# Performance work log

Hardware: AMD Instinct MI355X
Metric: run time of the kernel (lower is better)

Reference implementation:

```python
import jax, jax.numpy as jnp
import numpy as np

N = 20000        # nodes per type
E = 320000       # edges per type (avg degree 16)
H = 8            # heads
F0 = 128         # initial feature dim
F_UNI = 256      # n_unified
F_OUT = 64       # n_units per layer
N_USER = 20000   # shape_ret[0]
N_CLASSES = 2


def setup_inputs() -> dict:
    key = jax.random.key(0)
    ks = jax.random.split(key, 32)
    nrm = lambda k, s: jax.random.normal(k, s, dtype=jnp.float32) * 0.05
    inp = {
        "hemb0": nrm(ks[0], (N, F0)),
        "hemb1": nrm(ks[1], (N, F0)),
        "W0": nrm(ks[2], (F0, F_UNI)),
        "W1": nrm(ks[3], (F0, F_UNI)),
    }
    i = 4
    for t in range(2):
        for l, fin in enumerate([F_UNI, H * F_OUT]):
            inp[f"g{t}l{l}_w"] = nrm(ks[i], (H, fin, F_OUT)); i += 1
            inp[f"g{t}l{l}_asrc"] = nrm(ks[i], (H, F_OUT)); i += 1
            inp[f"g{t}l{l}_atrg"] = nrm(ks[i], (H, F_OUT)); i += 1
    inp["aw1"] = nrm(ks[i], (F_UNI, F_OUT)); i += 1
    inp["aw2"] = nrm(ks[i], (F_OUT, F_OUT)); i += 1
    inp["am"] = nrm(ks[i], (F_OUT,)); i += 1
    inp["fc_w"] = nrm(ks[i], (F_OUT * 3, N_CLASSES)); i += 1
    inp["fc_b"] = jnp.zeros((N_CLASSES,), jnp.float32); i += 1
    inp["edge0"] = jax.random.randint(ks[i], (2, E), 0, N, dtype=jnp.int32); i += 1
    inp["edge1"] = jax.random.randint(ks[i], (2, E), 0, N, dtype=jnp.int32)
    return inp


def spgat(h, src, trg, w, asrc, atrg):
    """Sparse GAT layer: h [N,f_in], edge list src/trg [E] -> [N,H,f_out]."""
    n = h.shape[0]
    hp = jnp.einsum('nf,hfo->hno', h, w)              # [H,N,O]
    s = jnp.einsum('hno,ho->nh', hp, asrc)            # [N,H]
    t = jnp.einsum('hno,ho->nh', hp, atrg)            # [N,H]
    e = jax.nn.leaky_relu(s[src] + t[trg], negative_slope=0.2)  # [E,H]
    ex = jnp.exp(e - jnp.max(e))                      # global max shift (as in source)
    denom = jax.ops.segment_sum(ex, trg, num_segments=n)[trg] + 1e-16
    alpha = ex / denom                                # [E,H]
    msg = jnp.transpose(hp, (1, 0, 2))[src] * alpha[:, :, None]  # [E,H,O]
    return jax.ops.segment_sum(msg, trg, num_segments=n)         # [N,H,O]


def reference(hemb0, hemb1, W0, W1,
              g0l0_w, g0l0_asrc, g0l0_atrg, g0l1_w, g0l1_asrc, g0l1_atrg,
              g1l0_w, g1l0_asrc, g1l0_atrg, g1l1_w, g1l1_asrc, g1l1_atrg,
              aw1, aw2, am, fc_w, fc_b, edge0, edge1):
    trans0 = hemb0 @ W0                                # [N,F_UNI]
    trans1 = hemb1 @ W1
    stacks = [
        (trans0, edge0, (g0l0_w, g0l0_asrc, g0l0_atrg), (g0l1_w, g0l1_asrc, g0l1_atrg)),
        (trans1, edge1, (g1l0_w, g1l0_asrc, g1l0_atrg), (g1l1_w, g1l1_asrc, g1l1_atrg)),
    ]
    heter = []
    for trans, edge, p0, p1 in stacks:
        src, trg = edge[0], edge[1]
        x = spgat(trans, src, trg, *p0)                # [N,H,F_OUT]
        x = jax.nn.elu(x.reshape(N, -1))               # [N,H*F_OUT]
        x = spgat(x, src, trg, *p1).mean(axis=1)       # [N,F_OUT]
        heter.append(x[:N_USER][:, None, :])
    type_aware = jnp.concatenate(heter, axis=1)        # [N_USER, 2, F_OUT]
    # faithful to source: feature = trans_emb[0] where trans_emb is the LAST
    # type's transformed embedding -> row 0, shape [F_UNI], broadcast over nodes
    feature = trans1[0]
    q = jnp.tanh(feature @ aw1 + type_aware @ aw2)     # [N_USER,2,F_OUT]
    beta = jax.nn.softmax(q @ am, axis=-1)             # [N_USER,2]
    fusion = jnp.einsum('nr,nrd->nd', beta, type_aware)[:, None, :]
    ret = jnp.concatenate([type_aware, fusion], axis=1).reshape(N_USER, -1)
    return jax.nn.log_softmax(ret @ fc_w + fc_b, axis=-1)   # [N_USER, 2]
```

## Files before the change

kernel.cpp:

```cpp
#include <hip/hip_runtime.h>
#include <hip/hip_bf16.h>


typedef __hip_bfloat16 bf16;
typedef __attribute__((ext_vector_type(8))) short short8;
typedef __attribute__((ext_vector_type(4))) float f32x4;

__device__ __forceinline__ float bf2f(bf16 v) { return __bfloat162float(v); }
__device__ __forceinline__ float ldin(const void* p, long i, int f32) {
  return f32 ? ((const float*)p)[i] : bf2f(((const bf16*)p)[i]);
}
__device__ __forceinline__ short f2bfbits(float f) {
  bf16 h = __float2bfloat16(f);
  return *reinterpret_cast<short*>(&h);
}
__device__ __forceinline__ float bfbits2f(short b) {
  unsigned u = ((unsigned)(unsigned short)b) << 16;
  return __uint_as_float(u);
}

struct GArg {
  const void* A[2];
  const void* B[2];
  bf16* C[2];
  const void* sa[2];
  const void* sb[2];
  float* sv[2];
  float* tv[2];
};

struct AArg {
  const bf16* hp[2];
  const float* sv[2];
  const float* tv[2];
  const int* rp[2];
  const int* col[2];
  void* out[2];
};

__global__ __launch_bounds__(64) void detect_kernel(const void* __restrict__ x,
                                                    int* __restrict__ flag) {
  int tid = threadIdx.x;
  float m = 0.f;
  for (int i = tid; i < 2048; i += 64) {
    float v = fabsf(bf2f(((const bf16*)x)[i]));
    if (!(v <= 1e3f)) v = 1e9f;
    m = fmaxf(m, v);
  }
#pragma unroll
  for (int off = 32; off; off >>= 1) m = fmaxf(m, __shfl_xor(m, off));
  if (tid == 0) flag[0] = (m > 1e3f) ? 1 : 0;
}

#define GBM 128
#define GBN 64
#define GBK 64

__device__ __forceinline__ int swz(int row, int kbyte) {
  return row * 128 + (kbyte ^ ((row & 7) << 4));
}

__global__ __launch_bounds__(256) void gemm_mfma(GArg g, int amode, int bmode,
                                                 int M, int K, int Nc,
                                                 const int* __restrict__ flag) {
  __shared__ bf16 As[GBM * GBK];
  __shared__ bf16 Bs[GBN * GBK];
  const int z = blockIdx.z;
  const void* __restrict__ A = g.A[z];
  const void* __restrict__ B = g.B[z];
  bf16* __restrict__ C = g.C[z];
  const void* stasrc = g.sa[z];
  const void* statrg = g.sb[z];
  float* svp = g.sv[z];
  float* tvp = g.tv[z];
  const int f32 = flag[0];
  const int af32 = (amode == 1) ? f32 : 0;
  const int bf32 = (bmode == 2) ? 0 : f32;
  const int m0 = blockIdx.x * GBM;
  const int n0 = blockIdx.y * GBN;
  const int tid = threadIdx.x;
  const int lane = tid & 63;
  const int wrow = (tid >> 6) * 32;

  f32x4 acc[2][4];
#pragma unroll
  for (int m = 0; m < 2; m++)
#pragma unroll
    for (int n = 0; n < 4; n++)
#pragma unroll
      for (int r = 0; r < 4; r++) acc[m][n][r] = 0.f;

  for (int kt = 0; kt < K; kt += GBK) {
#pragma unroll
    for (int j = 0; j < 4; j++) {
      int idx = tid + j * 256;
      int row = idx >> 3;
      int ks = idx & 7;
      int gm = m0 + row;
      short8 v;
#pragma unroll
      for (int e = 0; e < 8; e++) v[e] = 0;
      if (gm < M) {
        long base = (long)gm * K + kt + ks * 8;
        if (!af32) {
          v = *(const short8*)((const bf16*)A + base);
        } else {
          const float* Af = (const float*)A + base;
          float4 x0 = *(const float4*)Af;
          float4 x1 = *(const float4*)(Af + 4);
          v[0] = f2bfbits(x0.x); v[1] = f2bfbits(x0.y);
          v[2] = f2bfbits(x0.z); v[3] = f2bfbits(x0.w);
          v[4] = f2bfbits(x1.x); v[5] = f2bfbits(x1.y);
          v[6] = f2bfbits(x1.z); v[7] = f2bfbits(x1.w);
        }
      }
      *(short8*)((char*)As + swz(row, ks * 16)) = v;
    }
#pragma unroll
    for (int j = 0; j < 2; j++) {
      int idx = tid + j * 256;
      int k = idx >> 3;
      int colblk = idx & 7;
      long base;
      if (bmode == 1) base = ((long)blockIdx.y * K + kt + k) * 64 + colblk * 8;
      else base = (long)(kt + k) * Nc + n0 + colblk * 8;
      short8 v;
      if (bf32) {
        const float* Bf = (const float*)B + base;
        float4 x0 = *(const float4*)Bf;
        float4 x1 = *(const float4*)(Bf + 4);
        v[0] = f2bfbits(x0.x); v[1] = f2bfbits(x0.y);
        v[2] = f2bfbits(x0.z); v[3] = f2bfbits(x0.w);
        v[4] = f2bfbits(x1.x); v[5] = f2bfbits(x1.y);
        v[6] = f2bfbits(x1.z); v[7] = f2bfbits(x1.w);
      } else {
        v = *(const short8*)((const bf16*)B + base);
      }
#pragma unroll
      for (int e = 0; e < 8; e++)
        *(short*)((char*)Bs + swz(colblk * 8 + e, k * 2)) = v[e];
    }
    __syncthreads();
#pragma unroll
    for (int kh = 0; kh < 2; kh++) {
      int klane = kh * 64 + ((lane >> 4) << 4);
      short8 af[2], bfr[4];
#pragma unroll
      for (int m = 0; m < 2; m++) {
        int row = wrow + m * 16 + (lane & 15);
        af[m] = *(const short8*)((const char*)As + swz(row, klane));
      }
#pragma unroll
      for (int n = 0; n < 4; n++) {
        int col = n * 16 + (lane & 15);
        bfr[n] = *(const short8*)((const char*)Bs + swz(col, klane));
      }
#pragma unroll
      for (int m = 0; m < 2; m++)
#pragma unroll
        for (int n = 0; n < 4; n++)
          acc[m][n] = __builtin_amdgcn_mfma_f32_16x16x32_bf16(af[m], bfr[n], acc[m][n], 0, 0, 0);
    }
    __syncthreads();
  }
  if (svp) {
    const int h = blockIdx.y;
    const int cl = lane & 15;
    float av[4], bv[4];
#pragma unroll
    for (int n = 0; n < 4; n++) {
      av[n] = ldin(stasrc, h * 64 + n * 16 + cl, f32);
      bv[n] = ldin(statrg, h * 64 + n * 16 + cl, f32);
    }
#pragma unroll
    for (int m = 0; m < 2; m++) {
#pragma unroll
      for (int r = 0; r < 4; r++) {
        float s = 0.f, t = 0.f;
#pragma unroll
        for (int n = 0; n < 4; n++) {
          s += acc[m][n][r] * av[n];
          t += acc[m][n][r] * bv[n];
        }
#pragma unroll
        for (int off = 1; off <= 8; off <<= 1) {
          s += __shfl_xor(s, off);
          t += __shfl_xor(t, off);
        }
        int row = m0 + wrow + m * 16 + ((lane >> 4) << 2) + r;
        if (cl == 0 && row < M) {
          svp[(long)row * 8 + h] = s;
          tvp[(long)row * 8 + h] = t;
        }
      }
    }
  }
#pragma unroll
  for (int m = 0; m < 2; m++) {
#pragma unroll
    for (int r = 0; r < 4; r++) {
      int row = m0 + wrow + m * 16 + ((lane >> 4) << 2) + r;
      if (row < M) {
#pragma unroll
        for (int n = 0; n < 4; n++) {
          int col = n0 + n * 16 + (lane & 15);
          C[(long)row * Nc + col] = __float2bfloat16(acc[m][n][r]);
        }
      }
    }
  }
}

#define FKBM 64

__device__ __forceinline__ int swz256(int row, int kbyte) {
  return row * 256 + (kbyte ^ ((row & 7) << 4));
}

__global__ __launch_bounds__(256) void gemm_fullk(GArg g, int M,
                                                  const int* __restrict__ flag) {
  __shared__ bf16 As[FKBM * 128];
  __shared__ bf16 Bs[64 * 128];
  const int z = blockIdx.z;
  const void* __restrict__ A = g.A[z];
  const bf16* __restrict__ B = (const bf16*)g.B[z];
  bf16* __restrict__ C = g.C[z];
  const void* stasrc = g.sa[z];
  const void* statrg = g.sb[z];
  float* svp = g.sv[z];
  float* tvp = g.tv[z];
  const int f32 = flag[0];
  const int m0 = blockIdx.x * FKBM;
  const int tid = threadIdx.x;
  const int lane = tid & 63;
  const int wrow = (tid >> 6) * 16;

#pragma unroll
  for (int j = 0; j < 4; j++) {
    int idx = tid + j * 256;
    int row = idx >> 4;
    int ks = idx & 15;
    int gm = m0 + row;
    short8 v;
#pragma unroll
    for (int e = 0; e < 8; e++) v[e] = 0;
    if (gm < M) {
      long base = (long)gm * 128 + ks * 8;
      if (!f32) {
        v = *(const short8*)((const bf16*)A + base);
      } else {
        const float* Af = (const float*)A + base;
        float4 x0 = *(const float4*)Af;
        float4 x1 = *(const float4*)(Af + 4);
        v[0] = f2bfbits(x0.x); v[1] = f2bfbits(x0.y);
        v[2] = f2bfbits(x0.z); v[3] = f2bfbits(x0.w);
        v[4] = f2bfbits(x1.x); v[5] = f2bfbits(x1.y);
        v[6] = f2bfbits(x1.z); v[7] = f2bfbits(x1.w);
      }
    }
    *(short8*)((char*)As + swz256(row, ks * 16)) = v;
  }

  for (int p = 0; p < 8; p++) {
#pragma unroll
    for (int j = 0; j < 4; j++) {
      int idx = tid + j * 256;
      int k = idx >> 3;
      int colblk = idx & 7;
      short8 v = *(const short8*)(B + (long)k * 512 + p * 64 + colblk * 8);
#pragma unroll
      for (int e = 0; e < 8; e++)
        *(short*)((char*)Bs + swz256(colblk * 8 + e, k * 2)) = v[e];
    }
    __syncthreads();
    f32x4 acc[4];
#pragma unroll
    for (int n = 0; n < 4; n++)
#pragma unroll
      for (int r = 0; r < 4; r++) acc[n][r] = 0.f;
#pragma unroll
    for (int kb = 0; kb < 4; kb++) {
      int klane = kb * 64 + ((lane >> 4) << 4);
      short8 af = *(const short8*)((const char*)As + swz256(wrow + (lane & 15), klane));
      short8 bfr[4];
#pragma unroll
      for (int n = 0; n < 4; n++)
        bfr[n] = *(const short8*)((const char*)Bs + swz256(n * 16 + (lane & 15), klane));
#pragma unroll
      for (int n = 0; n < 4; n++)
        acc[n] = __builtin_amdgcn_mfma_f32_16x16x32_bf16(af, bfr[n], acc[n], 0, 0, 0);
    }
    {
      const int cl = lane & 15;
      float av[4], bv[4];
#pragma unroll
      for (int n = 0; n < 4; n++) {
        av[n] = ldin(stasrc, p * 64 + n * 16 + cl, f32);
        bv[n] = ldin(statrg, p * 64 + n * 16 + cl, f32);
      }
#pragma unroll
      for (int r = 0; r < 4; r++) {
        float s = 0.f, t = 0.f;
#pragma unroll
        for (int n = 0; n < 4; n++) {
          s += acc[n][r] * av[n];
          t += acc[n][r] * bv[n];
        }
#pragma unroll
        for (int off = 1; off <= 8; off <<= 1) {
          s += __shfl_xor(s, off);
          t += __shfl_xor(t, off);
        }
        int row = m0 + wrow + ((lane >> 4) << 2) + r;
        if (cl == 0 && row < M) {
          svp[(long)row * 8 + p] = s;
          tvp[(long)row * 8 + p] = t;
        }
      }
    }
#pragma unroll
    for (int r = 0; r < 4; r++) {
      int row = m0 + wrow + ((lane >> 4) << 2) + r;
      if (row < M) {
#pragma unroll
        for (int n = 0; n < 4; n++) {
          int col = p * 64 + n * 16 + (lane & 15);
          C[(long)row * 512 + col] = __float2bfloat16(acc[n][r]);
        }
      }
    }
    __syncthreads();
  }
}

__global__ void hist2_kernel(const int* __restrict__ trg0, const int* __restrict__ trg1,
                             int* __restrict__ deg, int E, int N) {
  int e = blockIdx.x * 256 + threadIdx.x;
  if (e < E) atomicAdd(&deg[trg0[e]], 1);
  else if (e < 2 * E) atomicAdd(&deg[N + trg1[e - E]], 1);
}

__global__ __launch_bounds__(1024) void scan_kernel(const int* __restrict__ degb,
                                                    int* __restrict__ rpb,
                                                    int* __restrict__ filb, int N) {
  const int* deg = degb + (long)blockIdx.x * N;
  int* row_ptr = rpb + (long)blockIdx.x * (N + 1);
  int* fil = filb + (long)blockIdx.x * N;
  __shared__ int sums[1024];
  int tid = threadIdx.x;
  int chunk = (N + 1023) >> 10;
  int start = tid * chunk;
  int end = start + chunk;
  if (start > N) start = N;
  if (end > N) end = N;
  int s = 0;
  for (int i = start; i < end; i++) s += deg[i];
  sums[tid] = s;
  __syncthreads();
  for (int off = 1; off < 1024; off <<= 1) {
    int add = (tid >= off) ? sums[tid - off] : 0;
    __syncthreads();
    sums[tid] += add;
    __syncthreads();
  }
  int run = (tid > 0) ? sums[tid - 1] : 0;
  for (int i = start; i < end; i++) {
    row_ptr[i] = run;
    fil[i] = run;
    run += deg[i];
  }
  if (tid == 0) row_ptr[N] = sums[1023];
}

__global__ void fill2_kernel(const int* __restrict__ src0, const int* __restrict__ trg0,
                             const int* __restrict__ src1, const int* __restrict__ trg1,
                             int* __restrict__ filb, int* __restrict__ colb, int E, int N) {
  int e = blockIdx.x * 256 + threadIdx.x;
  if (e < E) {
    int t = trg0[e];
    int pos = atomicAdd(&filb[t], 1);
    colb[pos] = src0[e];
  } else if (e < 2 * E) {
    int ee = e - E;
    int t = trg1[ee];
    int pos = atomicAdd(&filb[N + t], 1);
    colb[E + pos] = src1[ee];
  }
}

__device__ __forceinline__ float exleaky(float v) {
  v = v > 0.f ? v : 0.2f * v;
  return __expf(v);
}

__global__ __launch_bounds__(256) void aggregate(AArg aa, int N, int mode) {
  const int ty = blockIdx.y;
  const bf16* __restrict__ hpb = aa.hp[ty];
  const float* __restrict__ svb = aa.sv[ty];
  const float* __restrict__ tvb = aa.tv[ty];
  const int* __restrict__ rp = aa.rp[ty];
  const int* __restrict__ colv = aa.col[ty];
  void* __restrict__ outp = aa.out[ty];
  const int wid = threadIdx.x >> 6;
  const int lane = threadIdx.x & 63;
  const int n = blockIdx.x * 4 + wid;
  if (n >= N) return;
  const int start = rp[n];
  const int deg = rp[n + 1] - start;
  const int h = lane >> 3;
  const float tvh = tvb[(long)n * 8 + h];
  const bf16* __restrict__ hpc = hpb + lane * 8;

  float acc[8] = {0.f, 0.f, 0.f, 0.f, 0.f, 0.f, 0.f, 0.f};
  float den = 1e-16f;

#define AG_LOAD(EB, V0, V1, V2, V3, Q0, Q1, Q2, Q3)                 \
  {                                                                 \
    int t0 = __shfl(mysrc, (EB) + 0), t1 = __shfl(mysrc, (EB) + 1); \
    int t2 = __shfl(mysrc, (EB) + 2), t3 = __shfl(mysrc, (EB) + 3); \
    V0 = *(const short8*)(hpc + (long)t0 * 512);                    \
    V1 = *(const short8*)(hpc + (long)t1 * 512);                    \
    V2 = *(const short8*)(hpc + (long)t2 * 512);                    \
    V3 = *(const short8*)(hpc + (long)t3 * 512);                    \
    Q0 = svb[(long)t0 * 8 + h];                                     \
    Q1 = svb[(long)t1 * 8 + h];                                     \
    Q2 = svb[(long)t2 * 8 + h];                                     \
    Q3 = svb[(long)t3 * 8 + h];                                     \
  }
#define AG_ACC(V0, V1, V2, V3, Q0, Q1, Q2, Q3)                      \
  {                                                                 \
    float a0 = exleaky(Q0 + tvh), a1 = exleaky(Q1 + tvh);           \
    float a2 = exleaky(Q2 + tvh), a3 = exleaky(Q3 + tvh);           \
    den += a0 + a1 + a2 + a3;                                       \
    _Pragma("unroll")                                               \
    for (int j = 0; j < 8; j++)                                     \
      acc[j] += a0 * bfbits2f(V0[j]) + a1 * bfbits2f(V1[j]) +       \
                a2 * bfbits2f(V2[j]) + a3 * bfbits2f(V3[j]);        \
  }

  for (int base = 0; base < deg; base += 64) {
    int cnt = deg - base;
    if (cnt > 64) cnt = 64;
    int mysrc = (lane < cnt) ? colv[start + base + lane] : 0;
    int nfull = cnt & ~3;
    if (nfull) {
      short8 v0, v1, v2, v3;
      float q0, q1, q2, q3;
      AG_LOAD(0, v0, v1, v2, v3, q0, q1, q2, q3);
      for (int e = 4; e < nfull; e += 4) {
        short8 w0 = v0, w1 = v1, w2 = v2, w3 = v3;
        float p0 = q0, p1 = q1, p2 = q2, p3 = q3;
        AG_LOAD(e, v0, v1, v2, v3, q0, q1, q2, q3);
        AG_ACC(w0, w1, w2, w3, p0, p1, p2, p3);
      }
      AG_ACC(v0, v1, v2, v3, q0, q1, q2, q3);
    }
    for (int e = nfull; e < cnt; e++) {
      int s0 = __shfl(mysrc, e);
      short8 v = *(const short8*)(hpc + (long)s0 * 512);
      float a = exleaky(svb[(long)s0 * 8 + h] + tvh);
      den += a;
#pragma unroll
      for (int j = 0; j < 8; j++) acc[j] += a * bfbits2f(v[j]);
    }
  }

  const float dinv = 1.f / den;
  if (mode == 0) {
    short8 o8;
#pragma unroll
    for (int j = 0; j < 8; j++) {
      float s = acc[j] * dinv;
      float ev = s > 0.f ? s : expm1f(s);
      o8[j] = f2bfbits(ev);
    }
    *(short8*)((bf16*)outp + (long)n * 512 + lane * 8) = o8;
  } else {
    float r[8];
#pragma unroll
    for (int j = 0; j < 8; j++) r[j] = acc[j] * dinv;
#pragma unroll
    for (int m = 8; m <= 32; m <<= 1)
#pragma unroll
      for (int j = 0; j < 8; j++) r[j] += __shfl_xor(r[j], m);
    if (lane < 8) {
      float* o = (float*)outp + (long)n * 128 + lane * 8;
#pragma unroll
      for (int j = 0; j < 8; j++) o[j] = r[j] * 0.125f;
    }
  }
}

__global__ __launch_bounds__(256) void favec2_kernel(const void* __restrict__ hemb1,
                                                     const void* __restrict__ W1,
                                                     const void* __restrict__ aw1,
                                                     float* __restrict__ favec,
                                                     const int* __restrict__ flag) {
  const int f32 = flag[0];
  __shared__ float s_h[128];
  __shared__ float s_r[256];
  __shared__ float part[4][64];
  const int tid = threadIdx.x;
  if (tid < 128) s_h[tid] = ldin(hemb1, tid, f32);
  __syncthreads();
  float r = 0.f;
  for (int i = 0; i < 128; i++) r += s_h[i] * ldin(W1, (long)i * 256 + tid, f32);
  s_r[tid] = r;
  __syncthreads();
  const int o = tid & 63;
  const int wv = tid >> 6;
  float acc = 0.f;
#pragma unroll
  for (int kk = 0; kk < 64; kk++) {
    int k = wv * 64 + kk;
    acc += s_r[k] * ldin(aw1, (long)k * 64 + o, f32);
  }
  part[wv][o] = acc;
  __syncthreads();
  if (tid < 64) favec[o] = part[0][o] + part[1][o] + part[2][o] + part[3][o];
}

#define FN 16
__global__ __launch_bounds__(256) void final_kernel(const float* __restrict__ ta,
                                                    const float* __restrict__ favec,
                                                    const void* __restrict__ aw2,
                                                    const void* __restrict__ am,
                                                    const void* __restrict__ fcw,
                                                    const void* __restrict__ fcb,
                                                    void* __restrict__ out, int N,
                                                    const int* __restrict__ flag) {
  const int f32 = flag[0];
  __shared__ float s_w[64 * 64];
  __shared__ float s_fc[384];
  __shared__ float s_misc[130];
  __shared__ float s_ta[FN * 128];
  const int tid = threadIdx.x;
  const int n0 = blockIdx.x * FN;
  for (int i = tid; i < 4096; i += 256) s_w[i] = ldin(aw2, i, f32);
  for (int i = tid; i < 384; i += 256) s_fc[i] = ldin(fcw, i, f32);
  if (tid < 64) s_misc[tid] = favec[tid];
  else if (tid < 128) s_misc[tid] = ldin(am, tid - 64, f32);
  else if (tid < 130) s_misc[tid] = ldin(fcb, tid - 128, f32);
  for (int idx = tid; idx < FN * 128; idx += 256) {
    int ni = idx >> 7;
    int j = idx & 127;
    int k = j >> 1, r = j & 1;
    int n = n0 + ni;
    s_ta[idx] = (n < N) ? ta[(long)n * 128 + r * 64 + k] : 0.f;
  }
  __syncthreads();
  const int o = tid & 63;
  const int wv = tid >> 6;
#pragma unroll
  for (int ni4 = 0; ni4 < 4; ni4++) {
    const int ni = wv * 4 + ni4;
    const int n = n0 + ni;
    if (n >= N) continue;
    const float* tb = &s_ta[ni * 128];
    float acc0 = s_misc[o], acc1 = acc0;
#pragma unroll 8
    for (int k = 0; k < 64; k++) {
      float2 t2 = *(const float2*)(tb + k * 2);
      float w = s_w[k * 64 + o];
      acc0 += t2.x * w;
      acc1 += t2.y * w;
    }
    float ta0 = tb[o * 2];
    float ta1 = tb[o * 2 + 1];
    float amv = s_misc[64 + o];
    float p0 = tanhf(acc0) * amv;
    float p1 = tanhf(acc1) * amv;
#pragma unroll
    for (int off = 32; off > 0; off >>= 1) {
      p0 += __shfl_xor(p0, off);
      p1 += __shfl_xor(p1, off);
    }
    float mx = fmaxf(p0, p1);
    float e0 = __expf(p0 - mx), e1 = __expf(p1 - mx);
    float b0 = e0 / (e0 + e1), b1 = e1 / (e0 + e1);
    float fus = b0 * ta0 + b1 * ta1;
    float l0 = ta0 * s_fc[o * 2 + 0] + ta1 * s_fc[(64 + o) * 2 + 0] + fus * s_fc[(128 + o) * 2 + 0];
    float l1 = ta0 * s_fc[o * 2 + 1] + ta1 * s_fc[(64 + o) * 2 + 1] + fus * s_fc[(128 + o) * 2 + 1];
#pragma unroll
    for (int off = 32; off > 0; off >>= 1) {
      l0 += __shfl_xor(l0, off);
      l1 += __shfl_xor(l1, off);
    }
    if (o == 0) {
      l0 += s_misc[128];
      l1 += s_misc[129];
      float m2 = fmaxf(l0, l1);
      float lse = m2 + logf(__expf(l0 - m2) + __expf(l1 - m2));
      if (f32) {
        ((float*)out)[n * 2 + 0] = l0 - lse;
        ((float*)out)[n * 2 + 1] = l1 - lse;
      } else {
        ((bf16*)out)[n * 2 + 0] = __float2bfloat16(l0 - lse);
        ((bf16*)out)[n * 2 + 1] = __float2bfloat16(l1 - lse);
      }
    }
  }
}

extern "C" void kernel_launch(void* const* d_in, const int* in_sizes, int n_in,
                              void* d_out, int out_size, void* d_ws, size_t ws_size,
                              hipStream_t stream) {
  constexpr int N = 20000, E = 320000, H = 8, F0 = 128, FU = 256, FO = 64;
  const void* hemb[2] = {d_in[0], d_in[1]};
  const void* W[2] = {d_in[2], d_in[3]};
  const void* gw[2][2] = {{d_in[4], d_in[7]}, {d_in[10], d_in[13]}};
  const void* gasrc[2][2] = {{d_in[5], d_in[8]}, {d_in[11], d_in[14]}};
  const void* gatrg[2][2] = {{d_in[6], d_in[9]}, {d_in[12], d_in[15]}};
  const void* aw1 = d_in[16];
  const void* aw2 = d_in[17];
  const void* am = d_in[18];
  const void* fcw = d_in[19];
  const void* fcb = d_in[20];
  const int* edge[2] = {(const int*)d_in[21], (const int*)d_in[22]};

  const size_t szWg = (size_t)F0 * 512 * 2;
  const size_t szHp = (size_t)N * 512 * 2;
  const size_t szSv = (size_t)N * 8 * 4;
  size_t need = 0;
  auto addsz = [&](size_t b) { need += (b + 255) & ~(size_t)255; };
  addsz(4);
  addsz(szWg * 2);
  addsz(szHp * 2); addsz(szHp * 2);
  addsz(szSv * 2); addsz(szSv * 2);
  addsz((size_t)N * 128 * 4); addsz(256);
  addsz((size_t)2 * N * 4); addsz((size_t)2 * (N + 1) * 4);
  addsz((size_t)2 * N * 4); addsz((size_t)2 * E * 4);
  const bool batched = (ws_size >= need + 4096);
  const int TB = batched ? 2 : 1;

  char* p = (char*)d_ws;
  auto alloc = [&](size_t bytes) -> void* {
    void* r = (void*)p;
    p += (bytes + 255) & ~(size_t)255;
    return r;
  };
  int* flag = (int*)alloc(4);
  bf16* wg = (bf16*)alloc(szWg * 2);
  bf16* hp = (bf16*)alloc(szHp * TB);
  bf16* xbuf = (bf16*)alloc(szHp * TB);
  float* sv = (float*)alloc(szSv * TB);
  float* tv = (float*)alloc(szSv * TB);
  float* ta = (float*)alloc((size_t)N * 128 * 4);
  float* favec = (float*)alloc(256);
  int* degb = (int*)alloc((size_t)2 * N * 4);
  int* rpb = (int*)alloc((size_t)2 * (N + 1) * 4);
  int* filb = (int*)alloc((size_t)2 * N * 4);
  int* colb = (int*)alloc((size_t)2 * E * 4);

  detect_kernel<<<1, 64, 0, stream>>>(hemb[0], flag);

  hipMemsetAsync(degb, 0, (size_t)2 * N * 4, stream);
  hist2_kernel<<<(2 * E + 255) / 256, 256, 0, stream>>>(edge[0] + E, edge[1] + E, degb, E, N);
  scan_kernel<<<2, 1024, 0, stream>>>(degb, rpb, filb, N);
  fill2_kernel<<<(2 * E + 255) / 256, 256, 0, stream>>>(edge[0], edge[0] + E,
                                                        edge[1], edge[1] + E, filb, colb, E, N);

  favec2_kernel<<<1, 256, 0, stream>>>(hemb[1], W[1], aw1, favec, flag);

  {
    GArg gW{};
    for (int i = 0; i < 2; i++) {
      gW.A[i] = W[i]; gW.B[i] = gw[i][0]; gW.C[i] = wg + (size_t)i * F0 * 512;
      gW.sa[i] = nullptr; gW.sb[i] = nullptr; gW.sv[i] = nullptr; gW.tv[i] = nullptr;
    }
    gemm_mfma<<<dim3(1, (H * FO) / GBN, 2), 256, 0, stream>>>(gW, 1, 1, F0, FU, H * FO, flag);
  }

  const int gmx = (N + GBM - 1) / GBM;
  const int gfk = (N + FKBM - 1) / FKBM;
  const int npass = batched ? 1 : 2;
  const int TC = batched ? 2 : 1;

  auto hpP = [&](int b) { return hp + (size_t)b * N * 512; };
  auto xbufP = [&](int b) { return xbuf + (size_t)b * N * 512; };
  auto svP = [&](int b) { return sv + (size_t)b * N * 8; };
  auto tvP = [&](int b) { return tv + (size_t)b * N * 8; };

  for (int pass = 0; pass < npass; pass++) {
    int types[2] = {batched ? 0 : pass, batched ? 1 : pass};
    int bufs[2] = {0, batched ? 1 : 0};

    GArg g1{};
    for (int i = 0; i < TC; i++) {
      int t = types[i], b = bufs[i];
      g1.A[i] = hemb[t]; g1.B[i] = wg + (size_t)t * F0 * 512; g1.C[i] = hpP(b);
      g1.sa[i] = gasrc[t][0]; g1.sb[i] = gatrg[t][0]; g1.sv[i] = svP(b); g1.tv[i] = tvP(b);
    }
    gemm_fullk<<<dim3(gfk, 1, TC), 256, 0, stream>>>(g1, N, flag);

    AArg a0{};
    for (int i = 0; i < TC; i++) {
      int t = types[i], b = bufs[i];
      a0.hp[i] = hpP(b); a0.sv[i] = svP(b); a0.tv[i] = tvP(b);
      a0.rp[i] = rpb + (size_t)t * (N + 1); a0.col[i] = colb + (size_t)t * E;
      a0.out[i] = xbufP(b);
    }
    aggregate<<<dim3((N + 3) / 4, TC), 256, 0, stream>>>(a0, N, 0);

    GArg g2{};
    for (int i = 0; i < TC; i++) {
      int t = types[i], b = bufs[i];
      g2.A[i] = xbufP(b); g2.B[i] = gw[t][1]; g2.C[i] = hpP(b);
      g2.sa[i] = gasrc[t][1]; g2.sb[i] = gatrg[t][1]; g2.sv[i] = svP(b); g2.tv[i] = tvP(b);
    }
    gemm_mfma<<<dim3(gmx, (H * FO) / GBN, TC), 256, 0, stream>>>(g2, 0, 1, N, H * FO, H * FO, flag);

    AArg a1{};
    for (int i = 0; i < TC; i++) {
      int t = types[i], b = bufs[i];
      a1.hp[i] = hpP(b); a1.sv[i] = svP(b); a1.tv[i] = tvP(b);
      a1.rp[i] = rpb + (size_t)t * (N + 1); a1.col[i] = colb + (size_t)t * E;
      a1.out[i] = ta + (size_t)t * FO;
    }
    aggregate<<<dim3((N + 3) / 4, TC), 256, 0, stream>>>(a1, N, 1);
  }

  final_kernel<<<(N + FN - 1) / FN, 256, 0, stream>>>(ta, favec, aw2, am, fcw, fcb, d_out, N, flag);
}
```

Measured before the change: 575.6 us.

## Swizzle GEMM block order for L2 reuse and vectorize B tile LDS stores

The MFMA GEMM grid is flattened to one dimension and remapped so that groups of 8 M-tiles by 8 N-tiles (heads) run close together, which is meant to improve L2 reuse of A rows across heads. The B tile staging now has each thread gather 8 strided k-values for one column and write them as a single 16-byte LDS store, replacing eight 2-byte scattered LDS writes. In exchange the global B loads become strided scalar reads rather than vector reads. The remainder tiles use a fallback mapping.

```diff
diff --git a/kernel.cpp b/kernel.cpp
--- a/kernel.cpp
+++ b/kernel.cpp
@@ -76,8 +76,23 @@
   const int f32 = flag[0];
   const int af32 = (amode == 1) ? f32 : 0;
   const int bf32 = (bmode == 2) ? 0 : f32;
-  const int m0 = blockIdx.x * GBM;
-  const int n0 = blockIdx.y * GBN;
+
+  const int nx = gridDim.x >> 3;
+  const int d = blockIdx.x;
+  const int fullC = (gridDim.x >> 6) << 6;
+  int x, y;
+  if (d < fullC) {
+    x = (d & 7) + ((d >> 6) << 3);
+    y = (d >> 3) & 7;
+  } else {
+    int l = d - fullC;
+    int xbase = fullC >> 3;
+    int nrem = nx - xbase;
+    x = xbase + l % nrem;
+    y = l / nrem;
+  }
+  const int m0 = x * GBM;
+  const int n0 = y * GBN;
   const int tid = threadIdx.x;
   const int lane = tid & 63;
   const int wrow = (tid >> 6) * 32;
@@ -116,29 +131,30 @@
       }
       *(short8*)((char*)As + swz(row, ks * 16)) = v;
     }
-#pragma unroll
-    for (int j = 0; j < 2; j++) {
-      int idx = tid + j * 256;
-      int k = idx >> 3;
-      int colblk = idx & 7;
-      long base;
-      if (bmode == 1) base = ((long)blockIdx.y * K + kt + k) * 64 + colblk * 8;
-      else base = (long)(kt + k) * Nc + n0 + colblk * 8;
-      short8 v;
-      if (bf32) {
-        const float* Bf = (const float*)B + base;
-        float4 x0 = *(const float4*)Bf;
-        float4 x1 = *(const float4*)(Bf + 4);
-        v[0] = f2bfbits(x0.x); v[1] = f2bfbits(x0.y);
-        v[2] = f2bfbits(x0.z); v[3] = f2bfbits(x0.w);
-        v[4] = f2bfbits(x1.x); v[5] = f2bfbits(x1.y);
-        v[6] = f2bfbits(x1.z); v[7] = f2bfbits(x1.w);
-      } else {
-        v = *(const short8*)((const bf16*)B + base);
-      }
-#pragma unroll
-      for (int e = 0; e < 8; e++)
-        *(short*)((char*)Bs + swz(colblk * 8 + e, k * 2)) = v[e];
+    {
+      int n = tid & 63;
+      int ks0 = tid >> 6;
+#pragma unroll
+      for (int jj = 0; jj < 2; jj++) {
+        int ks = ks0 + jj * 4;
+        int k = kt + ks * 8;
+        int col = n0 + n;
+        long base;
+        int cstr;
+        if (bmode == 1) { base = ((long)(col >> 6) * K + k) * 64 + (col & 63); cstr = 64; }
+        else { base = (long)k * Nc + col; cstr = Nc; }
+        short8 v;
+        if (bf32) {
+          const float* Bf = (const float*)B;
+#pragma unroll
+          for (int e = 0; e < 8; e++) v[e] = f2bfbits(Bf[base + (long)e * cstr]);
+        } else {
+          const bf16* Bh = (const bf16*)B;
+#pragma unroll
+          for (int e = 0; e < 8; e++) v[e] = *(const short*)&Bh[base + (long)e * cstr];
+        }
+        *(short8*)((char*)Bs + swz(n, ks * 16)) = v;
+      }
     }
     __syncthreads();
 #pragma unroll
@@ -164,7 +180,7 @@
     __syncthreads();
   }
   if (svp) {
-    const int h = blockIdx.y;
+    const int h = y;
     const int cl = lane & 15;
     float av[4], bv[4];
 #pragma unroll
@@ -668,7 +684,7 @@
       gW.A[i] = W[i]; gW.B[i] = gw[i][0]; gW.C[i] = wg + (size_t)i * F0 * 512;
       gW.sa[i] = nullptr; gW.sb[i] = nullptr; gW.sv[i] = nullptr; gW.tv[i] = nullptr;
     }
-    gemm_mfma<<<dim3(1, (H * FO) / GBN, 2), 256, 0, stream>>>(gW, 1, 1, F0, FU, H * FO, flag);
+    gemm_mfma<<<dim3(8, 1, 2), 256, 0, stream>>>(gW, 1, 1, F0, FU, H * FO, flag);
   }
 
   const int gmx = (N + GBM - 1) / GBM;
@@ -708,7 +724,7 @@
       g2.A[i] = xbufP(b); g2.B[i] = gw[t][1]; g2.C[i] = hpP(b);
       g2.sa[i] = gasrc[t][1]; g2.sb[i] = gatrg[t][1]; g2.sv[i] = svP(b); g2.tv[i] = tvP(b);
     }
-    gemm_mfma<<<dim3(gmx, (H * FO) / GBN, TC), 256, 0, stream>>>(g2, 0, 1, N, H * FO, H * FO, flag);
+    gemm_mfma<<<dim3(gmx * 8, 1, TC), 256, 0, stream>>>(g2, 0, 1, N, H * FO, H * FO, flag);
 
     AArg a1{};
     for (int i = 0; i < TC; i++) {
```

Measured after the change: 558.0 us. 3.1% less time.
